# Kernel tuning notes

Measured on AMD Instinct MI355X. Metric: run time of the kernel, lower is better.

The kernel has to match this reference:

```python
import jax, jax.numpy as jnp
import numpy as np

SEQ, BATCH, IN, HID, LAYERS = 2048, 64, 256, 512, 2


def _uniform(key, shape, bound):
    return jax.random.uniform(key, shape, jnp.float32, -bound, bound)


def setup_inputs() -> dict:
    key = jax.random.key(0)
    ks = jax.random.split(key, 11)
    bound = 1.0 / np.sqrt(HID)
    inp = {
        "input": jax.random.normal(ks[0], (SEQ, BATCH, IN), jnp.float32),
        "h0": jnp.zeros((LAYERS, BATCH, HID), jnp.float32),
        "c0": jnp.zeros((LAYERS, BATCH, HID), jnp.float32),
        # layer 0 LSTM params (PyTorch gate order i,f,g,o stacked along 4H)
        "w_ih0": _uniform(ks[1], (4 * HID, IN), bound),
        "w_hh0": _uniform(ks[2], (4 * HID, HID), bound),
        "b_ih0": _uniform(ks[3], (4 * HID,), bound),
        "b_hh0": _uniform(ks[4], (4 * HID,), bound),
        # layer 1 LSTM params
        "w_ih1": _uniform(ks[5], (4 * HID, HID), bound),
        "w_hh1": _uniform(ks[6], (4 * HID, HID), bound),
        "b_ih1": _uniform(ks[7], (4 * HID,), bound),
        "b_hh1": _uniform(ks[8], (4 * HID,), bound),
        # output head: Linear(hidden_size, 1)
        "w_out": _uniform(ks[9], (1, HID), bound),
        "b_out": _uniform(ks[10], (1,), bound),
    }
    return inp


def _lstm_layer(x, h0, c0, w_ih, w_hh, b):
    # x: [S, B, D_in]; returns all hidden states [S, B, H]
    # Precompute input projections for the whole sequence (one big GEMM).
    x_proj = jnp.einsum("sbd,gd->sbg", x, w_ih) + b  # [S, B, 4H]

    def step(carry, xp):
        h, c = carry
        gates = xp + h @ w_hh.T  # [B, 4H]
        i, f, g, o = jnp.split(gates, 4, axis=-1)
        i = jax.nn.sigmoid(i)
        f = jax.nn.sigmoid(f)
        g = jnp.tanh(g)
        o = jax.nn.sigmoid(o)
        c = f * c + i * g
        h = o * jnp.tanh(c)
        return (h, c), h

    _, hs = jax.lax.scan(step, (h0, c0), x_proj)
    return hs


def reference(input, h0, c0, w_ih0, w_hh0, b_ih0, b_hh0,
              w_ih1, w_hh1, b_ih1, b_hh1, w_out, b_out):
    h = _lstm_layer(input, h0[0], c0[0], w_ih0, w_hh0, b_ih0 + b_hh0)
    h = _lstm_layer(h, h0[1], c0[1], w_ih1, w_hh1, b_ih1 + b_hh1)
    out = jnp.einsum("sbh,oh->sbo", h, w_out) + b_out  # [S, B, 1]
    return jax.nn.sigmoid(out)
```

## Files before the change

kernel.cpp:

```cpp
#include <hip/hip_runtime.h>
#include <hip/hip_bf16.h>


#define SEQ    2048
#define BATCH  64
#define NIN    256
#define HID    512
#define NWGL   32
#define UPW    16
#define NWG    65
#define NSTEP  (SEQ + 3)

#define RING      65536
#define FLAGS_OFF 0
#define H0_OFF    8192
#define H1_OFF    (H0_OFF + 3 * RING)

typedef __bf16 bf16x8 __attribute__((ext_vector_type(8)));
typedef float  f32x4  __attribute__((ext_vector_type(4)));
typedef unsigned int u32;
typedef unsigned int u32x4 __attribute__((ext_vector_type(4)));

__device__ __forceinline__ float sigf(float x) { return 1.0f / (1.0f + __expf(-x)); }
__device__ __forceinline__ float tanh_f(float x) { return 2.0f / (1.0f + __expf(-2.0f * x)) - 1.0f; }

__device__ __forceinline__ bf16x8 cvt8(const float* __restrict__ p) {
    bf16x8 r;
#pragma unroll
    for (int i = 0; i < 8; ++i) r[i] = (__bf16)p[i];
    return r;
}

__device__ __forceinline__ u32x4 llc_ld16(const void* p) {
    u32x4 r;
    asm volatile("global_load_dwordx4 %0, %1, off sc0 sc1" : "=v"(r) : "v"(p));
    return r;
}
__device__ __forceinline__ void llc_st16(void* p, u32x4 v) {
    asm volatile("global_store_dwordx4 %0, %1, off sc0 sc1" :: "v"(p), "v"(v) : "memory");
}
__device__ __forceinline__ void llc_st4(void* p, u32 v) {
    asm volatile("global_store_dword %0, %1, off sc0 sc1" :: "v"(p), "v"(v) : "memory");
}
__device__ __forceinline__ u32 llc_ld4_wait(const void* p) {
    u32 r;
    asm volatile("global_load_dword %0, %1, off sc0 sc1\n\ts_waitcnt vmcnt(0)"
                 : "=v"(r) : "v"(p) : "memory");
    return r;
}
__device__ __forceinline__ void waitcnt_vm0()  { asm volatile("s_waitcnt vmcnt(0)"  ::: "memory"); }
__device__ __forceinline__ void waitcnt_vm32() { asm volatile("s_waitcnt vmcnt(32)" ::: "memory"); }

__device__ __forceinline__ void poll_ge(const u32* p, u32 tgt) {
    while (llc_ld4_wait(p) < tgt) __builtin_amdgcn_s_sleep(1);
}

__device__ __forceinline__ void stage_issue(const char* __restrict__ slot, int tid, u32x4 (&t)[16]) {
    const int batch = tid >> 2, j0 = tid & 3;
#pragma unroll
    for (int i = 0; i < 16; ++i)
        t[i] = llc_ld16(slot + batch * 1024 + (j0 + 4 * i) * 16);
}
__device__ __forceinline__ void stage_commit(char* __restrict__ buf, int tid, u32x4 (&t)[16]) {
    const int batch = tid >> 2, j0 = tid & 3;
#pragma unroll
    for (int i = 0; i < 16; ++i)
        *(u32x4*)(buf + (j0 + 4 * i) * 1024 + batch * 16) = t[i];
}

__global__ void prep_kernel(char* __restrict__ ws) {
    const int idx = blockIdx.x * blockDim.x + threadIdx.x;
    const int stride = gridDim.x * blockDim.x;
    for (int i = idx; i < 1024 / 4; i += stride)
        llc_st4(ws + FLAGS_OFF + 4 * i, 0u);
    char* s0 = ws + H0_OFF + 2 * RING;
    char* s1 = ws + H1_OFF + 2 * RING;
    for (int i = idx; i < RING / 4; i += stride) {
        llc_st4(s0 + 4 * i, 0u);
        llc_st4(s1 + 4 * i, 0u);
    }
}

__global__ void __launch_bounds__(256, 1)
lstm_kernel(const float* __restrict__ xin,
            const float* __restrict__ wih0, const float* __restrict__ whh0,
            const float* __restrict__ bih0, const float* __restrict__ bhh0,
            const float* __restrict__ wih1, const float* __restrict__ whh1,
            const float* __restrict__ bih1, const float* __restrict__ bhh1,
            const float* __restrict__ wout, const float* __restrict__ bout,
            float* __restrict__ out, char* __restrict__ ws)
{
    extern __shared__ char smem[];
    u32*  flags = (u32*)(ws + FLAGS_OFF);
    char* h0r   = ws + H0_OFF;
    char* h1r   = ws + H1_OFF;

    const int wg  = blockIdx.x;
    const int tid = threadIdx.x;
    const int lane = tid & 63;

    if (wg == 64) {
        float* wsm  = (float*)smem;
        float* psum = (float*)(smem + 2048);
        for (int i = tid; i < HID; i += 256) wsm[i] = wout[i];
        const float bo = bout[0];
        const int hb = tid >> 2, kq = tid & 3;
        for (int v = 0; v < NSTEP; ++v) {
            if (v >= 3) {
                poll_ge(flags + 64 + (lane & 31), (u32)v);
                __syncthreads();
                const char* hrow = h1r + (size_t)(v % 3) * RING + hb * 1024 + kq * 256;
                u32x4 tv[16];
#pragma unroll
                for (int i = 0; i < 16; ++i) tv[i] = llc_ld16(hrow + i * 16);
                waitcnt_vm0();
                __syncthreads();
                if (tid == 0) llc_st4((void*)(flags + 96), (u32)(v + 1));
                const float* wrow = wsm + kq * 128;
                float s = 0.0f;
#pragma unroll
                for (int i = 0; i < 16; ++i) {
                    bf16x8 hv = __builtin_bit_cast(bf16x8, tv[i]);
#pragma unroll
                    for (int e = 0; e < 8; ++e) s += (float)hv[e] * wrow[i * 8 + e];
                }
                psum[tid] = s;
                __syncthreads();
                if (tid < 64) {
                    float d = psum[4 * tid] + psum[4 * tid + 1] + psum[4 * tid + 2] + psum[4 * tid + 3] + bo;
                    out[(size_t)(v - 3) * BATCH + tid] = sigf(d);
                }
                __syncthreads();
            } else {
                if (tid == 0) llc_st4((void*)(flags + 96), (u32)(v + 1));
            }
        }
        return;
    }

    const int layer = wg >> 5;
    const int wgL   = wg & 31;
    const int wave  = tid >> 6;
    const int quad  = lane >> 4;
    const int l16   = lane & 15;
    const int gh    = wave >> 1;
    const int bh    = wave & 1;
    const int bcol0 = 16 * (2 * bh + 0) + l16;
    const int bcol1 = 16 * (2 * bh + 1) + l16;

    char* bufB = smem;
    char* epil = smem;

    float bias[2][4];
    {
        const float* bi = layer ? bih1 : bih0;
        const float* bb = layer ? bhh1 : bhh0;
#pragma unroll
        for (int t = 0; t < 2; ++t) {
            const int u = wgL * UPW + 4 * (2 * gh + t) + quad;
#pragma unroll
            for (int q = 0; q < 4; ++q) bias[t][q] = bi[q * HID + u] + bb[q * HID + u];
        }
    }
    float cst[2][2] = {{0.f, 0.f}, {0.f, 0.f}};
    f32x4 acc[2][2];

    auto gemm16 = [&](bf16x8 (&W)[2][16]) {
#pragma unroll
        for (int ks = 0; ks < 16; ++ks) {
            bf16x8 B0 = *(const bf16x8*)(bufB + ((ks * 4 + quad) << 10) + (bcol0 << 4));
            bf16x8 B1 = *(const bf16x8*)(bufB + ((ks * 4 + quad) << 10) + (bcol1 << 4));
#pragma unroll
            for (int t = 0; t < 2; ++t) {
                acc[t][0] = __builtin_amdgcn_mfma_f32_16x16x32_bf16(W[t][ks], B0, acc[t][0], 0, 0, 0);
                acc[t][1] = __builtin_amdgcn_mfma_f32_16x16x32_bf16(W[t][ks], B1, acc[t][1], 0, 0, 0);
            }
        }
    };

    auto epilogue = [&](char* wslot, u32* myflag, int v) {
#pragma unroll
        for (int t = 0; t < 2; ++t) {
            const int uloc = 4 * (2 * gh + t) + quad;
#pragma unroll
            for (int b = 0; b < 2; ++b) {
                const float gi = acc[t][b][0] + bias[t][0];
                const float gf = acc[t][b][1] + bias[t][1];
                const float gg = acc[t][b][2] + bias[t][2];
                const float go = acc[t][b][3] + bias[t][3];
                const float cc = sigf(gf) * cst[t][b] + sigf(gi) * tanh_f(gg);
                cst[t][b] = cc;
                const float hh = sigf(go) * tanh_f(cc);
                const int bb = (b == 0) ? bcol0 : bcol1;
                *(unsigned short*)(epil + bb * 32 + uloc * 2) =
                    __builtin_bit_cast(unsigned short, (__bf16)hh);
            }
        }
        __syncthreads();
        if (tid < 128) {
            const int bb = tid >> 1, half = tid & 1;
            u32x4 val = *(const u32x4*)(epil + bb * 32 + half * 16);
            llc_st16(wslot + bb * 1024 + wgL * 32 + half * 16, val);
        }
        waitcnt_vm0();
        __syncthreads();
        if (tid == 0) llc_st4((void*)myflag, (u32)(v + 1));
    };

    if (layer == 0) {
        bf16x8 wIH[2][8], wHH[2][16];
        {
#pragma unroll
            for (int t = 0; t < 2; ++t) {
                const int r = 16 * (2 * gh + t) + l16;
                const int u = wgL * UPW + (r >> 2);
                const int q = r & 3;
                const float* srcI = wih0 + (size_t)(q * HID + u) * NIN + quad * 8;
                const float* srcH = whh0 + (size_t)(q * HID + u) * HID + quad * 8;
#pragma unroll
                for (int ks = 0; ks < 8; ++ks)  wIH[t][ks] = cvt8(srcI + ks * 32);
#pragma unroll
                for (int ks = 0; ks < 16; ++ks) wHH[t][ks] = cvt8(srcH + ks * 32);
            }
        }
        u32x4 xpre[2][8][2];
        auto issue_x = [&](int xv) {
            const float* xb  = xin + (size_t)xv * BATCH * NIN;
            const float* xr0 = xb + (size_t)bcol0 * NIN + quad * 8;
            const float* xr1 = xb + (size_t)bcol1 * NIN + quad * 8;
#pragma unroll
            for (int ks = 0; ks < 8; ++ks) {
                xpre[0][ks][0] = llc_ld16(xr0 + ks * 32);
                xpre[0][ks][1] = llc_ld16(xr0 + ks * 32 + 4);
                xpre[1][ks][0] = llc_ld16(xr1 + ks * 32);
                xpre[1][ks][1] = llc_ld16(xr1 + ks * 32 + 4);
            }
        };
        issue_x(0);
        waitcnt_vm0();

        for (int v = 0; v < NSTEP; ++v) {
            if (v < SEQ) {
#pragma unroll
                for (int t = 0; t < 2; ++t)
#pragma unroll
                    for (int b = 0; b < 2; ++b) acc[t][b] = (f32x4){0.f, 0.f, 0.f, 0.f};
#pragma unroll
                for (int ks = 0; ks < 8; ++ks) {
                    bf16x8 B0, B1;
                    {
                        f32x4 lo = __builtin_bit_cast(f32x4, xpre[0][ks][0]);
                        f32x4 hi = __builtin_bit_cast(f32x4, xpre[0][ks][1]);
#pragma unroll
                        for (int e = 0; e < 4; ++e) { B0[e] = (__bf16)lo[e]; B0[4 + e] = (__bf16)hi[e]; }
                        lo = __builtin_bit_cast(f32x4, xpre[1][ks][0]);
                        hi = __builtin_bit_cast(f32x4, xpre[1][ks][1]);
#pragma unroll
                        for (int e = 0; e < 4; ++e) { B1[e] = (__bf16)lo[e]; B1[4 + e] = (__bf16)hi[e]; }
                    }
#pragma unroll
                    for (int t = 0; t < 2; ++t) {
                        acc[t][0] = __builtin_amdgcn_mfma_f32_16x16x32_bf16(wIH[t][ks], B0, acc[t][0], 0, 0, 0);
                        acc[t][1] = __builtin_amdgcn_mfma_f32_16x16x32_bf16(wIH[t][ks], B1, acc[t][1], 0, 0, 0);
                    }
                }
                poll_ge(flags + lane, (u32)v);
                __syncthreads();
                u32x4 t16[16];
                stage_issue(h0r + (size_t)((v + 2) % 3) * RING, tid, t16);
                issue_x(v + 1 < SEQ ? v + 1 : SEQ - 1);
                waitcnt_vm32();
                stage_commit(bufB, tid, t16);
                __syncthreads();
                gemm16(wHH);
                __syncthreads();
                epilogue(h0r + (size_t)(v % 3) * RING, flags + wgL, v);
            } else {
                if (tid == 0) llc_st4((void*)(flags + wgL), (u32)(v + 1));
            }
        }
    } else {
        bf16x8 wIH[2][16], wHH[2][16];
        {
#pragma unroll
            for (int t = 0; t < 2; ++t) {
                const int r = 16 * (2 * gh + t) + l16;
                const int u = wgL * UPW + (r >> 2);
                const int q = r & 3;
                const float* srcI = wih1 + (size_t)(q * HID + u) * HID + quad * 8;
                const float* srcH = whh1 + (size_t)(q * HID + u) * HID + quad * 8;
#pragma unroll
                for (int ks = 0; ks < 16; ++ks) { wIH[t][ks] = cvt8(srcI + ks * 32); wHH[t][ks] = cvt8(srcH + ks * 32); }
            }
        }
        for (int v = 0; v < NSTEP; ++v) {
            if (v >= 2 && v < SEQ + 2) {
                poll_ge(flags + (lane & 31), (u32)(v - 1));
                __syncthreads();
                {
                    u32x4 t16[16];
                    stage_issue(h0r + (size_t)((v + 1) % 3) * RING, tid, t16);
                    waitcnt_vm0();
                    stage_commit(bufB, tid, t16);
                }
                __syncthreads();
                if (tid == 0) llc_st4((void*)(flags + 32 + wgL), (u32)(v + 1));
#pragma unroll
                for (int t = 0; t < 2; ++t)
#pragma unroll
                    for (int b = 0; b < 2; ++b) acc[t][b] = (f32x4){0.f, 0.f, 0.f, 0.f};
                gemm16(wIH);
                {
                    int idx; u32 tgt;
                    if (lane < 32) { idx = 64 + lane; tgt = (u32)v; }
                    else           { idx = 96;        tgt = (u32)(v - 1); }
                    poll_ge(flags + idx, tgt);
                }
                __syncthreads();
                {
                    u32x4 t16[16];
                    stage_issue(h1r + (size_t)(v % 3) * RING, tid, t16);
                    waitcnt_vm0();
                    stage_commit(bufB, tid, t16);
                }
                __syncthreads();
                gemm16(wHH);
                __syncthreads();
                epilogue(h1r + (size_t)((v + 1) % 3) * RING, flags + 64 + wgL, v);
            } else {
                if (tid == 0) {
                    llc_st4((void*)(flags + 32 + wgL), (u32)(v + 1));
                    llc_st4((void*)(flags + 64 + wgL), (u32)(v + 1));
                }
            }
        }
    }
}

extern "C" void kernel_launch(void* const* d_in, const int* in_sizes, int n_in,
                              void* d_out, int out_size, void* d_ws, size_t ws_size,
                              hipStream_t stream) {
    (void)in_sizes; (void)n_in; (void)out_size; (void)ws_size;
    const float* xin  = (const float*)d_in[0];
    const float* wih0 = (const float*)d_in[3];
    const float* whh0 = (const float*)d_in[4];
    const float* bih0 = (const float*)d_in[5];
    const float* bhh0 = (const float*)d_in[6];
    const float* wih1 = (const float*)d_in[7];
    const float* whh1 = (const float*)d_in[8];
    const float* bih1 = (const float*)d_in[9];
    const float* bhh1 = (const float*)d_in[10];
    const float* wout = (const float*)d_in[11];
    const float* bout = (const float*)d_in[12];
    float* out = (float*)d_out;
    char* ws = (char*)d_ws;

    hipLaunchKernelGGL(prep_kernel, dim3(64), dim3(256), 0, stream, ws);
    hipLaunchKernelGGL(lstm_kernel, dim3(NWG), dim3(256), 65536, stream,
                       xin, wih0, whh0, bih0, bhh0,
                       wih1, whh1, bih1, bhh1,
                       wout, bout, out, ws);
}
```

Measured before the change: 16.08 ms.

## Merge layer-1 polls and prefetch both hidden-state slots before GEMMs

Layer-1 workgroups now wait once for every dependency, including the layer-0 h, their own previous h1 and the output-head consumer flag. They then issue loads for both hidden-state slots together, so the h1 load overlaps the input GEMM instead of requiring a second poll and barrier. Layer 0 moves its poll and h-load issue ahead of the x-projection MFMAs so those loads overlap the compute. Polling is restricted to a subset of threads, and x loads drop the sc0/sc1 LLC-coherent bits so they can be served from cache. The added work is more live registers and a stricter wait on the h1 dependency before the input GEMM starts.

Result: faster. 15.67 ms (median of 2 runs) (-2.6%).

```diff
diff --git a/kernel.cpp b/kernel.cpp
--- a/kernel.cpp
+++ b/kernel.cpp
@@ -36,6 +36,11 @@
     asm volatile("global_load_dwordx4 %0, %1, off sc0 sc1" : "=v"(r) : "v"(p));
     return r;
 }
+__device__ __forceinline__ u32x4 cached_ld16(const void* p) {
+    u32x4 r;
+    asm volatile("global_load_dwordx4 %0, %1, off" : "=v"(r) : "v"(p));
+    return r;
+}
 __device__ __forceinline__ void llc_st16(void* p, u32x4 v) {
     asm volatile("global_store_dwordx4 %0, %1, off sc0 sc1" :: "v"(p), "v"(v) : "memory");
 }
@@ -49,6 +54,7 @@
     return r;
 }
 __device__ __forceinline__ void waitcnt_vm0()  { asm volatile("s_waitcnt vmcnt(0)"  ::: "memory"); }
+__device__ __forceinline__ void waitcnt_vm16() { asm volatile("s_waitcnt vmcnt(16)" ::: "memory"); }
 __device__ __forceinline__ void waitcnt_vm32() { asm volatile("s_waitcnt vmcnt(32)" ::: "memory"); }
 
 __device__ __forceinline__ void poll_ge(const u32* p, u32 tgt) {
@@ -107,7 +113,7 @@
         const int hb = tid >> 2, kq = tid & 3;
         for (int v = 0; v < NSTEP; ++v) {
             if (v >= 3) {
-                poll_ge(flags + 64 + (lane & 31), (u32)v);
+                if (tid < 32) poll_ge(flags + 64 + tid, (u32)v);
                 __syncthreads();
                 const char* hrow = h1r + (size_t)(v % 3) * RING + hb * 1024 + kq * 256;
                 u32x4 tv[16];
@@ -230,10 +236,10 @@
             const float* xr1 = xb + (size_t)bcol1 * NIN + quad * 8;
 #pragma unroll
             for (int ks = 0; ks < 8; ++ks) {
-                xpre[0][ks][0] = llc_ld16(xr0 + ks * 32);
-                xpre[0][ks][1] = llc_ld16(xr0 + ks * 32 + 4);
-                xpre[1][ks][0] = llc_ld16(xr1 + ks * 32);
-                xpre[1][ks][1] = llc_ld16(xr1 + ks * 32 + 4);
+                xpre[0][ks][0] = cached_ld16(xr0 + ks * 32);
+                xpre[0][ks][1] = cached_ld16(xr0 + ks * 32 + 4);
+                xpre[1][ks][0] = cached_ld16(xr1 + ks * 32);
+                xpre[1][ks][1] = cached_ld16(xr1 + ks * 32 + 4);
             }
         };
         issue_x(0);
@@ -241,10 +247,14 @@
 
         for (int v = 0; v < NSTEP; ++v) {
             if (v < SEQ) {
+                if (tid < 64) poll_ge(flags + tid, (u32)v);
+                __syncthreads();
 #pragma unroll
                 for (int t = 0; t < 2; ++t)
 #pragma unroll
                     for (int b = 0; b < 2; ++b) acc[t][b] = (f32x4){0.f, 0.f, 0.f, 0.f};
+                u32x4 t16[16];
+                stage_issue(h0r + (size_t)((v + 2) % 3) * RING, tid, t16);
 #pragma unroll
                 for (int ks = 0; ks < 8; ++ks) {
                     bf16x8 B0, B1;
@@ -264,10 +274,6 @@
                         acc[t][1] = __builtin_amdgcn_mfma_f32_16x16x32_bf16(wIH[t][ks], B1, acc[t][1], 0, 0, 0);
                     }
                 }
-                poll_ge(flags + lane, (u32)v);
-                __syncthreads();
-                u32x4 t16[16];
-                stage_issue(h0r + (size_t)((v + 2) % 3) * RING, tid, t16);
                 issue_x(v + 1 < SEQ ? v + 1 : SEQ - 1);
                 waitcnt_vm32();
                 stage_commit(bufB, tid, t16);
@@ -295,14 +301,18 @@
         }
         for (int v = 0; v < NSTEP; ++v) {
             if (v >= 2 && v < SEQ + 2) {
-                poll_ge(flags + (lane & 31), (u32)(v - 1));
-                __syncthreads();
-                {
-                    u32x4 t16[16];
-                    stage_issue(h0r + (size_t)((v + 1) % 3) * RING, tid, t16);
-                    waitcnt_vm0();
-                    stage_commit(bufB, tid, t16);
-                }
+                if (tid < 64) {
+                    if (lane < 32) poll_ge(flags + 64 + lane, (u32)v);
+                    else           poll_ge(flags + (lane - 32), (u32)(v - 1));
+                } else if (tid == 64) {
+                    poll_ge(flags + 96, (u32)(v - 1));
+                }
+                __syncthreads();
+                u32x4 ta[16], tb[16];
+                stage_issue(h0r + (size_t)((v + 1) % 3) * RING, tid, ta);
+                stage_issue(h1r + (size_t)(v % 3) * RING, tid, tb);
+                waitcnt_vm16();
+                stage_commit(bufB, tid, ta);
                 __syncthreads();
                 if (tid == 0) llc_st4((void*)(flags + 32 + wgL), (u32)(v + 1));
 #pragma unroll
@@ -310,19 +320,9 @@
 #pragma unroll
                     for (int b = 0; b < 2; ++b) acc[t][b] = (f32x4){0.f, 0.f, 0.f, 0.f};
                 gemm16(wIH);
-                {
-                    int idx; u32 tgt;
-                    if (lane < 32) { idx = 64 + lane; tgt = (u32)v; }
-                    else           { idx = 96;        tgt = (u32)(v - 1); }
-                    poll_ge(flags + idx, tgt);
-                }
-                __syncthreads();
-                {
-                    u32x4 t16[16];
-                    stage_issue(h1r + (size_t)(v % 3) * RING, tid, t16);
-                    waitcnt_vm0();
-                    stage_commit(bufB, tid, t16);
-                }
+                __syncthreads();
+                waitcnt_vm0();
+                stage_commit(bufB, tid, tb);
                 __syncthreads();
                 gemm16(wHH);
                 __syncthreads();
```
